# Kernel tuning notes

Measured on AMD Instinct MI355X. Metric: run time of the kernel, lower is better.

The kernel has to match this reference:

```python
import jax, jax.numpy as jnp
import numpy as np

# ---- static config (mirrors init_kwargs) ----
B, T, N, FIN = 32, 12, 500, 2
U, ND, ED = 32, 32, 2            # factor dim, node_dim, edge_dim
NRES, NDIL, NSKIP, NEND, NPRED = 32, 32, 256, 512, 12
NBLOCKS, NLAYERS, KS, ORDER = 4, 2, 2, 2
L = NBLOCKS * NLAYERS
DILATIONS = [2 ** i for _ in range(NBLOCKS) for i in range(NLAYERS)]
RF = NBLOCKS * (KS - 1) * (2 ** NLAYERS - 1) + 1  # receptive field = 13
GCIN = (ORDER * ED + 1) * NDIL                     # graph-conv concat channels = 160
BN_EPS = 1e-5


def conv1x1(x, w, b):
    # x: [B,C,N,T], w: [O,C]
    return jnp.einsum('bcnt,oc->bont', x, w) + b[None, :, None, None]


def dilated_tconv(x, w, b, d):
    # valid dilated conv along time. x: [B,C,N,T], w: [O,C,K]
    k_sz = w.shape[-1]
    t_out = x.shape[-1] - (k_sz - 1) * d
    out = jnp.einsum('bcnt,oc->bont', x[..., 0:t_out], w[..., 0])
    for k in range(1, k_sz):
        out = out + jnp.einsum('bcnt,oc->bont', x[..., k * d:k * d + t_out], w[..., k])
    return out + b[None, :, None, None]


def graph_conv(x, supports, w, b):
    # x: [B,C,N,T]; supports: [E,N,N]; diffusion over node axis (dim 2)
    out = [x]
    for e in range(supports.shape[0]):
        x1 = jnp.einsum('bcvt,vw->bcwt', x, supports[e])
        out.append(x1)
        for _ in range(ORDER - 1):
            x1 = jnp.einsum('bcvt,vw->bcwt', x1, supports[e])
            out.append(x1)
    h = jnp.concatenate(out, axis=1)  # [B,GCIN,N,T]
    return conv1x1(h, w, b)


def batchnorm(x, g, bta):
    m = x.mean(axis=(0, 2, 3), keepdims=True)
    v = ((x - m) ** 2).mean(axis=(0, 2, 3), keepdims=True)
    return (x - m) * jax.lax.rsqrt(v + BN_EPS) * g[None, :, None, None] + bta[None, :, None, None]


def _forward(inputs, factor, map_w, map_b, a1w, a1b, a2w, a2b, a3w, a3b,
             enter_w, enter_b, filt_w, filt_b, gate_w, gate_b,
             skp_w, skp_b, gc_w, gc_b, bn_g, bn_b, o1w, o1b, o2w, o2b):
    n = factor.shape[0]
    # ---- adaptive supports ----
    v = jax.nn.relu(factor @ map_w + map_b)                      # [N, ND]
    src = jnp.broadcast_to(v[None, :, :], (n, n, v.shape[1]))    # src[i,j]=v[j]
    dst = jnp.broadcast_to(v[:, None, :], (n, n, v.shape[1]))    # dst[i,j]=v[i]
    h = jnp.concatenate([src, dst], axis=-1)                     # [N,N,2*ND]
    h = jax.nn.relu(h @ a1w + a1b)
    h = jax.nn.relu(h @ a2w + a2b)
    adj = (h @ a3w + a3b).transpose(2, 0, 1)                     # [E,N,N]
    adj = jax.nn.softmax(adj, axis=2)
    supports = jnp.maximum(adj, jnp.eye(n, dtype=adj.dtype))
    # ---- input split ----
    static = jnp.einsum('btuf,pu->btpf', jnp.einsum('btnf,nu->btuf', inputs, factor), factor)
    x = jnp.concatenate([static, inputs - static], axis=-1)      # [B,T,N,2F]
    x = x.transpose(0, 3, 2, 1)                                  # [B,2F,N,T]
    t_in = x.shape[-1]
    if t_in < RF:
        x = jnp.pad(x, ((0, 0), (0, 0), (0, 0), (RF - t_in, 0)))
    x = conv1x1(x, enter_w, enter_b)                             # [B,NRES,N,RF]
    skip = jnp.zeros((x.shape[0], NSKIP, n, x.shape[-1]), dtype=x.dtype)
    # ---- stacked ST layers ----
    for i, d in enumerate(DILATIONS):
        residual = x
        f = jnp.tanh(dilated_tconv(x, filt_w[i], filt_b[i], d))
        g = jax.nn.sigmoid(dilated_tconv(x, gate_w[i], gate_b[i], d))
        x = f * g                                                # [B,NDIL,N,T']
        s = conv1x1(x, skp_w[i], skp_b[i])
        skip = skip[..., skip.shape[-1] - s.shape[-1]:] + s
        x = graph_conv(x, supports, gc_w[i], gc_b[i])
        x = x + residual[..., residual.shape[-1] - x.shape[-1]:]
        x = batchnorm(x, bn_g[i], bn_b[i])
    # ---- output head ----
    y = jax.nn.relu(skip)
    y = jax.nn.relu(conv1x1(y, o1w, o1b))
    y = conv1x1(y, o2w, o2b)                                     # [B,NPRED,N,1]
    return y, supports


def setup_inputs() -> dict:
    key = jax.random.key(0)
    ks = jax.random.split(key, 16)
    def w(i, shape, s=0.02):
        return s * jax.random.normal(ks[i], shape, dtype=jnp.float32)
    return {
        'inputs': jax.random.normal(ks[0], (B, T, N, FIN), dtype=jnp.float32),
        'factor': 0.05 * jax.random.normal(ks[1], (N, U), dtype=jnp.float32),
        'map_w': w(2, (U, ND), 0.1), 'map_b': jnp.zeros((ND,), jnp.float32),
        'a1w': w(3, (2 * ND, 2 * ND), 0.1), 'a1b': jnp.zeros((2 * ND,), jnp.float32),
        'a2w': w(4, (2 * ND, ND), 0.1), 'a2b': jnp.zeros((ND,), jnp.float32),
        'a3w': w(5, (ND, ED), 0.1), 'a3b': jnp.zeros((ED,), jnp.float32),
        'enter_w': w(6, (NRES, 2 * FIN)), 'enter_b': jnp.zeros((NRES,), jnp.float32),
        'filt_w': w(7, (L, NDIL, NRES, KS)), 'filt_b': jnp.zeros((L, NDIL), jnp.float32),
        'gate_w': w(8, (L, NDIL, NRES, KS)), 'gate_b': jnp.zeros((L, NDIL), jnp.float32),
        'skp_w': w(9, (L, NSKIP, NDIL)), 'skp_b': jnp.zeros((L, NSKIP), jnp.float32),
        'gc_w': w(10, (L, NRES, GCIN)), 'gc_b': jnp.zeros((L, NRES), jnp.float32),
        'bn_g': jnp.ones((L, NRES), jnp.float32), 'bn_b': jnp.zeros((L, NRES), jnp.float32),
        'o1w': w(11, (NEND, NSKIP)), 'o1b': jnp.zeros((NEND,), jnp.float32),
        'o2w': w(12, (NPRED, NEND)), 'o2b': jnp.zeros((NPRED,), jnp.float32),
    }


def reference(inputs, factor, map_w, map_b, a1w, a1b, a2w, a2b, a3w, a3b,
              enter_w, enter_b, filt_w, filt_b, gate_w, gate_b,
              skp_w, skp_b, gc_w, gc_b, bn_g, bn_b, o1w, o1b, o2w, o2b):
    return _forward(inputs, factor, map_w, map_b, a1w, a1b, a2w, a2b, a3w, a3b,
                    enter_w, enter_b, filt_w, filt_b, gate_w, gate_b,
                    skp_w, skp_b, gc_w, gc_b, bn_g, bn_b, o1w, o1b, o2w, o2b)
```

## Files before the change

kernel.cpp:

```cpp
#include <hip/hip_runtime.h>
#include <math.h>

#define BB 32
#define TT 12
#define NN 500
#define UU 32
#define CC 32
#define NSKIPC 256
#define NENDC 512
#define NPREDC 12
#define TX 13
#define TG 12
#define QS 384
#define VS 512
#define BNN (BB*NN)
#define DSZ (BNN*TG*CC)
#define BN_EPS 1e-5f

#define OFF_V      0u
#define OFF_ADJ    16000u
#define OFF_ASRC   516000u
#define OFF_ADST   548000u
#define OFF_PROJ   580000u
#define OFF_STAT   582048u
#define OFF_PART   582560u
#define OFF_BSUM   774560u
#define OFF_X      774816u
#define OFF_XN     7430816u
#define OFF_D      14086816u
#define OFF_GBF    38662816u
#define OFF_GLB    41734816u
#define OFF_GT     43782816u
#define OFF_ST     46928544u
#define OFF_SB     47190688u
#define OFF_ST2    47452832u
#define OFF_WSTB   47714976u
#define OFF_O1WB   47747744u
#define OFF_SKV    47813280u
#define OFF_Y1B    49861280u

typedef __attribute__((ext_vector_type(8))) short bf16x8;
typedef __attribute__((ext_vector_type(4))) float f32x4;

__device__ inline unsigned short f2bf(float f) {
  union { float f; unsigned u; } x; x.f = f;
  unsigned r = x.u + 0x7FFFu + ((x.u >> 16) & 1u);
  return (unsigned short)(r >> 16);
}
__device__ inline float bf2f(short s) {
  union { float f; unsigned u; } x;
  x.u = ((unsigned)(unsigned short)s) << 16;
  return x.f;
}
__device__ inline int pk2(float a, float b) {
  return (int)((unsigned)f2bf(a) | ((unsigned)f2bf(b) << 16));
}
__device__ inline bf16x8 pack8(f32x4 a, f32x4 b) {
  union { int i[4]; bf16x8 v; } u;
  u.i[0]=pk2(a.x,a.y); u.i[1]=pk2(a.z,a.w);
  u.i[2]=pk2(b.x,b.y); u.i[3]=pk2(b.z,b.w);
  return u.v;
}
__device__ inline f32x4 reluadd(f32x4 a, f32x4 b) {
  f32x4 r;
  r.x=fmaxf(a.x+b.x,0.f); r.y=fmaxf(a.y+b.y,0.f);
  r.z=fmaxf(a.z+b.z,0.f); r.w=fmaxf(a.w+b.w,0.f);
  return r;
}


__global__ void k_v(const float* __restrict__ factor, const float* __restrict__ map_w,
                    const float* __restrict__ map_b, float* __restrict__ v) {
  int n = blockIdx.x; int d = threadIdx.x;
  __shared__ float fr[UU];
  fr[d] = factor[n*UU + d];
  __syncthreads();
  float acc = map_b[d];
#pragma unroll
  for (int u=0;u<UU;u++) acc += fr[u]*map_w[u*32+d];
  v[n*32+d] = fmaxf(acc, 0.f);
}

__global__ void k_asrc2(const float* __restrict__ v, const float* __restrict__ a1w,
                        const float* __restrict__ a1b,
                        float* __restrict__ asrc, float* __restrict__ adst) {
  int n = blockIdx.x; int o = threadIdx.x;
  __shared__ float vn[32];
  if (o < 32) vn[o] = v[n*32+o];
  __syncthreads();
  float s = 0.f, dst = a1b[o];
#pragma unroll
  for (int u=0;u<32;u++){ s += vn[u]*a1w[u*64+o]; dst += vn[u]*a1w[(32+u)*64+o]; }
  asrc[n*64+o] = s;
  adst[n*64+o] = dst;
}

__global__ __launch_bounds__(256) void k_pair3(const float* __restrict__ asrc,
    const float* __restrict__ adst, const float* __restrict__ a2w,
    const float* __restrict__ a2b, const float* __restrict__ a3w,
    const float* __restrict__ a3b, float* __restrict__ adj) {
  int i = blockIdx.x;
  int tid = threadIdx.x;
  int wid = tid>>6, lane = tid&63;
  int lm = lane&15, g = lane>>4, lk8 = g*8;
  int jb = blockIdx.y*256 + wid*64;
  bf16x8 wf[2][2];
#pragma unroll
  for (int ks=0;ks<2;ks++)
#pragma unroll
    for (int nh=0;nh<2;nh++){
      int n = nh*16+lm;
      f32x4 lo, hi;
      lo.x=a2w[(ks*32+lk8+0)*32+n]; lo.y=a2w[(ks*32+lk8+1)*32+n];
      lo.z=a2w[(ks*32+lk8+2)*32+n]; lo.w=a2w[(ks*32+lk8+3)*32+n];
      hi.x=a2w[(ks*32+lk8+4)*32+n]; hi.y=a2w[(ks*32+lk8+5)*32+n];
      hi.z=a2w[(ks*32+lk8+6)*32+n]; hi.w=a2w[(ks*32+lk8+7)*32+n];
      wf[ks][nh] = pack8(lo, hi);
    }
  float b20 = a2b[lm], b21 = a2b[16+lm];
  float w3e0n0 = a3w[lm*2],      w3e1n0 = a3w[lm*2+1];
  float w3e0n1 = a3w[(16+lm)*2], w3e1n1 = a3w[(16+lm)*2+1];
  float b30 = a3b[0], b31 = a3b[1];
  const float* dp = adst + i*64;
  f32x4 d00 = *(const f32x4*)(dp + lk8);
  f32x4 d01 = *(const f32x4*)(dp + lk8 + 4);
  f32x4 d10 = *(const f32x4*)(dp + 32 + lk8);
  f32x4 d11 = *(const f32x4*)(dp + 32 + lk8 + 4);
#pragma unroll
  for (int mg=0; mg<4; mg++){
    int j = jb + mg*16 + lm;
    int jc = j < 500 ? j : 0;
    const float* ap = asrc + jc*64;
    f32x4 s00=*(const f32x4*)(ap+lk8),    s01=*(const f32x4*)(ap+lk8+4);
    f32x4 s10=*(const f32x4*)(ap+32+lk8), s11=*(const f32x4*)(ap+32+lk8+4);
    bf16x8 a0 = pack8(reluadd(s00,d00), reluadd(s01,d01));
    bf16x8 a1 = pack8(reluadd(s10,d10), reluadd(s11,d11));
    f32x4 acc0 = {b20,b20,b20,b20};
    f32x4 acc1 = {b21,b21,b21,b21};
    acc0 = __builtin_amdgcn_mfma_f32_16x16x32_bf16(a0, wf[0][0], acc0, 0,0,0);
    acc0 = __builtin_amdgcn_mfma_f32_16x16x32_bf16(a1, wf[1][0], acc0, 0,0,0);
    acc1 = __builtin_amdgcn_mfma_f32_16x16x32_bf16(a0, wf[0][1], acc1, 0,0,0);
    acc1 = __builtin_amdgcn_mfma_f32_16x16x32_bf16(a1, wf[1][1], acc1, 0,0,0);
    float e0[4], e1[4];
#pragma unroll
    for (int r=0;r<4;r++){
      float h2a = fmaxf(acc0[r],0.f), h2b = fmaxf(acc1[r],0.f);
      e0[r] = h2a*w3e0n0 + h2b*w3e0n1;
      e1[r] = h2a*w3e1n0 + h2b*w3e1n1;
    }
#pragma unroll
    for (int off=1; off<16; off<<=1){
#pragma unroll
      for (int r=0;r<4;r++){ e0[r]+=__shfl_xor(e0[r],off); e1[r]+=__shfl_xor(e1[r],off); }
    }
    if (lm==0){
      int j4 = jb + mg*16 + g*4;
      if (j4 < 500){
        f32x4 v0={e0[0]+b30,e0[1]+b30,e0[2]+b30,e0[3]+b30};
        f32x4 v1={e1[0]+b31,e1[1]+b31,e1[2]+b31,e1[3]+b31};
        *(f32x4*)(adj + i*500 + j4) = v0;
        *(f32x4*)(adj + 250000 + i*500 + j4) = v1;
      }
    }
  }
}

__global__ __launch_bounds__(256) void k_softmax(const float* __restrict__ adj,
    float* __restrict__ sup_out) {
  int row = blockIdx.x;
  int e = row/NN, i = row%NN;
  const float* a = adj + e*250000 + i*NN;
  __shared__ float red[64];
  float m = -1e30f;
  for (int j=threadIdx.x;j<NN;j+=256) m = fmaxf(m, a[j]);
#pragma unroll
  for (int off=32; off; off>>=1) m = fmaxf(m, __shfl_down(m, off));
  int lane = threadIdx.x & 63, wid = threadIdx.x >> 6;
  if (lane==0) red[wid]=m;
  __syncthreads();
  if (threadIdx.x==0){ float mm=red[0]; for(int w=1;w<4;w++) mm=fmaxf(mm,red[w]); red[32]=mm; }
  __syncthreads();
  m = red[32];
  float s=0.f;
  for (int j=threadIdx.x;j<NN;j+=256) s += __expf(a[j]-m);
#pragma unroll
  for (int off=32; off; off>>=1) s += __shfl_down(s, off);
  if (lane==0) red[wid]=s;
  __syncthreads();
  if (threadIdx.x==0){ float ss=0; for(int w=0;w<4;w++) ss+=red[w]; red[33]=ss; }
  __syncthreads();
  float inv = 1.f/red[33];
  for (int j=threadIdx.x;j<NN;j+=256) {
    float val = __expf(a[j]-m)*inv;
    if (j==i) val = 1.f;
    sup_out[e*250000 + i*NN + j] = val;
  }
}

__global__ __launch_bounds__(256) void k_tposeS(const float* __restrict__ sup,
    short* __restrict__ ST, short* __restrict__ SB) {
  __shared__ float ts[64][68];
  int e = blockIdx.z;
  int v0 = blockIdx.x*64, w0 = blockIdx.y*64;
  int tid = threadIdx.x;
  int vv = tid>>2, wc = (tid&3)*16;
  bool vok = (v0+vv) < 500;
#pragma unroll
  for (int c=0;c<4;c++){
    f32x4 val = {0,0,0,0};
    int wg = w0 + wc + c*4;
    if (vok && wg < 500) val = *(const f32x4*)(sup + e*250000 + (size_t)(v0+vv)*500 + wg);
    *(f32x4*)&ts[vv][wc + c*4] = val;
    int2 pv; pv.x = pk2(val.x, val.y); pv.y = pk2(val.z, val.w);
    *(int2*)(SB + (size_t)e*(512*512) + (size_t)(v0+vv)*VS + wg) = pv;
  }
  __syncthreads();
  int w = tid>>2, vc = (tid&3)*16;
  unsigned short u[16];
#pragma unroll
  for (int j=0;j<16;j++) u[j] = f2bf(ts[vc+j][w]);
  int4 o0, o1;
  o0.x = u[0]|(u[1]<<16);  o0.y = u[2]|(u[3]<<16);
  o0.z = u[4]|(u[5]<<16);  o0.w = u[6]|(u[7]<<16);
  o1.x = u[8]|(u[9]<<16);  o1.y = u[10]|(u[11]<<16);
  o1.z = u[12]|(u[13]<<16); o1.w = u[14]|(u[15]<<16);
  short* op = ST + (size_t)e*(512*512) + (size_t)(w0+w)*VS + v0 + vc;
  *(int4*)(op) = o0;
  *(int4*)(op+8) = o1;
}

__global__ __launch_bounds__(256) void k_ssq(const short* __restrict__ SB,
    const short* __restrict__ ST, short* __restrict__ ST2) {
  __shared__ __align__(16) short As[64*72];
  __shared__ __align__(16) short Bs[64*72];
  int e = blockIdx.z;
  int u0 = blockIdx.x*64, w0 = blockIdx.y*64;
  const short* Ab = SB + (size_t)e*(512*512);
  const short* Bb = ST + (size_t)e*(512*512);
  int tid = threadIdx.x;
  int row = tid>>2, col = (tid&3)*16;
  const short* ap = Ab + (size_t)(u0+row)*VS + col;
  const short* bp = Bb + (size_t)(w0+row)*VS + col;
  f32x4 ra0 = *(const f32x4*)(ap);
  f32x4 ra1 = *(const f32x4*)(ap+8);
  f32x4 rb0 = *(const f32x4*)(bp);
  f32x4 rb1 = *(const f32x4*)(bp+8);
  int wid = tid>>6, lane = tid&63;
  int wr = wid>>1, wc = wid&1;
  int lm = lane&15, lk = (lane>>4)*8;
  f32x4 acc[2][2] = {};
  short* aw = As + row*72 + col;
  short* bw = Bs + row*72 + col;
  for (int kk=0; kk<8; kk++) {
    __syncthreads();
    *(f32x4*)(aw) = ra0; *(f32x4*)(aw+8) = ra1;
    *(f32x4*)(bw) = rb0; *(f32x4*)(bw+8) = rb1;
    __syncthreads();
    if (kk < 7) {
      const short* ap2 = ap + (kk+1)*64;
      const short* bp2 = bp + (kk+1)*64;
      ra0 = *(const f32x4*)(ap2); ra1 = *(const f32x4*)(ap2+8);
      rb0 = *(const f32x4*)(bp2); rb1 = *(const f32x4*)(bp2+8);
    }
#pragma unroll
    for (int ks=0; ks<2; ks++) {
      bf16x8 af0 = *(const bf16x8*)(As + (wr*32 + lm)*72 + ks*32 + lk);
      bf16x8 af1 = *(const bf16x8*)(As + (wr*32 + 16 + lm)*72 + ks*32 + lk);
      bf16x8 bq0 = *(const bf16x8*)(Bs + (wc*32 + lm)*72 + ks*32 + lk);
      bf16x8 bq1 = *(const bf16x8*)(Bs + (wc*32 + 16 + lm)*72 + ks*32 + lk);
      acc[0][0] = __builtin_amdgcn_mfma_f32_16x16x32_bf16(af0, bq0, acc[0][0], 0,0,0);
      acc[0][1] = __builtin_amdgcn_mfma_f32_16x16x32_bf16(af0, bq1, acc[0][1], 0,0,0);
      acc[1][0] = __builtin_amdgcn_mfma_f32_16x16x32_bf16(af1, bq0, acc[1][0], 0,0,0);
      acc[1][1] = __builtin_amdgcn_mfma_f32_16x16x32_bf16(af1, bq1, acc[1][1], 0,0,0);
    }
  }
#pragma unroll
  for (int fm=0; fm<2; fm++) {
    int u4 = u0 + wr*32 + fm*16 + (lane>>4)*4;
#pragma unroll
    for (int fn=0; fn<2; fn++) {
      int w = w0 + wc*32 + fn*16 + lm;
      f32x4 v4 = acc[fm][fn];
      int2 pv; pv.x = pk2(v4.x, v4.y); pv.y = pk2(v4.z, v4.w);
      *(int2*)(ST2 + (size_t)e*(512*512) + (size_t)w*VS + u4) = pv;
    }
  }
}

__global__ __launch_bounds__(256) void k_tposeGb(const short* __restrict__ Gbf,
    short* __restrict__ GT, int qmax) {
  __shared__ __align__(16) short ts[64][72];
  int b = blockIdx.z;
  int v0 = blockIdx.x*64, q0 = blockIdx.y*64;
  int tid = threadIdx.x;
  int vv = tid>>2, qc = (tid&3)*16;
  bool ok = ((v0+vv) < 500) && ((q0+qc) < qmax);
  int4 z4 = {0,0,0,0};
  int4 i0 = z4, i1 = z4;
  if (ok){
    const short* gp = Gbf + (size_t)(b*NN + v0+vv)*QS + q0 + qc;
    i0 = *(const int4*)(gp);
    i1 = *(const int4*)(gp+8);
  }
  *(int4*)&ts[vv][qc] = i0;
  *(int4*)&ts[vv][qc+8] = i1;
  __syncthreads();
  int q = tid>>2, vc = (tid&3)*16;
  if (q0 + q < qmax) {
    unsigned short u[16];
#pragma unroll
    for (int j=0;j<16;j++) u[j] = (unsigned short)ts[vc+j][q];
    int4 o0, o1;
    o0.x = u[0]|(u[1]<<16);  o0.y = u[2]|(u[3]<<16);
    o0.z = u[4]|(u[5]<<16);  o0.w = u[6]|(u[7]<<16);
    o1.x = u[8]|(u[9]<<16);  o1.y = u[10]|(u[11]<<16);
    o1.z = u[12]|(u[13]<<16); o1.w = u[14]|(u[15]<<16);
    short* op = GT + ((size_t)b*QS + q0+q)*VS + v0 + vc;
    *(int4*)(op) = o0;
    *(int4*)(op+8) = o1;
  }
}

__global__ __launch_bounds__(256) void k_hop2(const short* __restrict__ ST,
    const short* __restrict__ ST2, const short* __restrict__ GT,
    short* __restrict__ Dout, int qmax, int qt) {
  __shared__ __align__(16) short LB[2*128*72];
  short* As = LB;
  short* Bs = LB + 128*72;
  int nwg = gridDim.x;
  int w = (blockIdx.x & 7) * (nwg >> 3) + (blockIdx.x >> 3);
  int x = w & 3; w >>= 2;
  int y = w % qt; w /= qt;
  int sel = w & 3; int b = w >> 2;
  int e = sel >> 1, hop = sel & 1;
  int w0 = x*128, q0 = y*128;
  const short* Ab = (hop ? ST2 : ST) + (size_t)e*(512*512) + (size_t)w0*VS;
  const short* Bb = GT + (size_t)b*(QS*VS) + (size_t)q0*VS;
  int tid = threadIdx.x;
  int row = tid>>2, col = (tid&3)*16;
  const short* ap0 = Ab + (size_t)row*VS + col;
  const short* ap1 = ap0 + (size_t)64*VS;
  const short* bp0 = Bb + (size_t)row*VS + col;
  const short* bp1 = bp0 + (size_t)64*VS;
  f32x4 a00=*(const f32x4*)ap0, a01=*(const f32x4*)(ap0+8);
  f32x4 a10=*(const f32x4*)ap1, a11=*(const f32x4*)(ap1+8);
  f32x4 b00=*(const f32x4*)bp0, b01=*(const f32x4*)(bp0+8);
  f32x4 b10=*(const f32x4*)bp1, b11=*(const f32x4*)(bp1+8);
  int wid = tid>>6, lane = tid&63;
  int wr = wid>>1, wc = wid&1;
  int lm = lane&15, lk = (lane>>4)*8;
  f32x4 acc[4][4] = {};
  short* aw0 = As + row*72 + col; short* aw1 = aw0 + 64*72;
  short* bw0 = Bs + row*72 + col; short* bw1 = bw0 + 64*72;
  for (int kk=0; kk<8; kk++) {
    __syncthreads();
    *(f32x4*)(aw0) = a00; *(f32x4*)(aw0+8) = a01;
    *(f32x4*)(aw1) = a10; *(f32x4*)(aw1+8) = a11;
    *(f32x4*)(bw0) = b00; *(f32x4*)(bw0+8) = b01;
    *(f32x4*)(bw1) = b10; *(f32x4*)(bw1+8) = b11;
    __syncthreads();
    if (kk < 7) {
      int o = (kk+1)*64;
      a00=*(const f32x4*)(ap0+o); a01=*(const f32x4*)(ap0+o+8);
      a10=*(const f32x4*)(ap1+o); a11=*(const f32x4*)(ap1+o+8);
      b00=*(const f32x4*)(bp0+o); b01=*(const f32x4*)(bp0+o+8);
      b10=*(const f32x4*)(bp1+o); b11=*(const f32x4*)(bp1+o+8);
    }
#pragma unroll
    for (int ks=0; ks<2; ks++) {
      bf16x8 af[4], bq[4];
#pragma unroll
      for (int fm=0;fm<4;fm++) af[fm] = *(const bf16x8*)(As + (wr*64+fm*16+lm)*72 + ks*32 + lk);
#pragma unroll
      for (int fn=0;fn<4;fn++) bq[fn] = *(const bf16x8*)(Bs + (wc*64+fn*16+lm)*72 + ks*32 + lk);
#pragma unroll
      for (int fm=0;fm<4;fm++)
#pragma unroll
        for (int fn=0;fn<4;fn++)
          acc[fm][fn] = __builtin_amdgcn_mfma_f32_16x16x32_bf16(af[fm], bq[fn], acc[fm][fn], 0,0,0);
    }
  }
  __syncthreads();
#pragma unroll
  for (int fm=0; fm<4; fm++){
    int rr = wr*64 + fm*16 + (lane>>4)*4;
#pragma unroll
    for (int fn=0; fn<4; fn++){
      int cc = wc*64 + fn*16 + lm;
      f32x4 v4 = acc[fm][fn];
      LB[(rr+0)*136 + cc] = (short)f2bf(v4.x);
      LB[(rr+1)*136 + cc] = (short)f2bf(v4.y);
      LB[(rr+2)*136 + cc] = (short)f2bf(v4.z);
      LB[(rr+3)*136 + cc] = (short)f2bf(v4.w);
    }
  }
  __syncthreads();
  short* Ob = Dout + (size_t)sel*DSZ + (size_t)b*(NN*QS);
#pragma unroll
  for (int pass=0; pass<8; pass++){
    int rr = pass*16 + (tid>>4);
    int cc = (tid&15)*8;
    int wg = w0 + rr, qg = q0 + cc;
    if (wg < 500 && qg < qmax){
      int4 vv = *(const int4*)(LB + rr*136 + cc);
      *(int4*)(Ob + (size_t)wg*QS + qg) = vv;
    }
  }
}


__global__ void k_proj(const float* __restrict__ inputs, const float* __restrict__ factor,
                       float* __restrict__ proj) {
  int bt = blockIdx.x;
  __shared__ float xin[NN*2];
  for (int idx=threadIdx.x; idx<NN*2; idx+=64) xin[idx] = inputs[bt*NN*2 + idx];
  __syncthreads();
  int u = threadIdx.x>>1, f = threadIdx.x&1;
  float acc=0.f;
  for (int n=0;n<NN;n++) acc += xin[n*2+f]*factor[n*UU+u];
  proj[bt*64 + u*2+f] = acc;
}

__global__ __launch_bounds__(256) void k_enter(const float* __restrict__ inputs,
    const float* __restrict__ factor, const float* __restrict__ proj,
    const float* __restrict__ ew, const float* __restrict__ eb, float* __restrict__ X) {
  int idx = blockIdx.x*256+threadIdx.x;
  if (idx >= BB*NN*TX) return;
  int t = idx % TX; int n = (idx/TX)%NN; int b = idx/(TX*NN);
  float x4[4]={0.f,0.f,0.f,0.f};
  if (t>0) {
    int tt=t-1;
    float s0=0.f,s1=0.f;
    const float* pr = proj + (b*TT+tt)*64;
    const float* fr = factor + n*UU;
#pragma unroll
    for(int u=0;u<UU;u++){ s0 += pr[u*2]*fr[u]; s1 += pr[u*2+1]*fr[u]; }
    float i0 = inputs[((b*TT+tt)*NN+n)*2];
    float i1 = inputs[((b*TT+tt)*NN+n)*2+1];
    x4[0]=s0; x4[1]=s1; x4[2]=i0-s0; x4[3]=i1-s1;
  }
  float* xp = X + ((size_t)(b*NN+n)*TX + t)*CC;
#pragma unroll
  for(int o=0;o<CC;o++){
    xp[o] = eb[o] + ew[o*4]*x4[0] + ew[o*4+1]*x4[1] + ew[o*4+2]*x4[2] + ew[o*4+3]*x4[3];
  }
}


__global__ __launch_bounds__(256) void k_gated3(const float* __restrict__ X,
    short* __restrict__ Gbf, short* __restrict__ Glb,
    const float* __restrict__ fw, const float* __restrict__ fb,
    const float* __restrict__ gw, const float* __restrict__ gb,
    const float* __restrict__ stat, int use_stat, int d, int t_out, int lidx) {
  __shared__ __align__(16) short As[64*72];
  __shared__ __align__(16) short Wb[64*72];
  __shared__ float scs[32], shs[32];
  int tid = threadIdx.x;
  if (tid < 32) {
    scs[tid] = use_stat ? stat[tid] : 1.0f;
    shs[tid] = use_stat ? stat[32 + tid] : 0.0f;
  }
  for (int i = tid; i < 2048; i += 256) {
    int o = i >> 6, k = i & 63;
    Wb[o*72 + k]      = (short)f2bf(fw[i]);
    Wb[(32+o)*72 + k] = (short)f2bf(gw[i]);
  }
  __syncthreads();
  int m0 = blockIdx.x * 64;
  {
    int mm = tid & 63;
    int kb = (tid >> 6) * 16;
    int c0 = kb >> 1;
    int m = m0 + mm;
    int bn = m / t_out, t = m - bn * t_out;
    const float* xr = X + (size_t)bn * (TX * CC);
    float4 a0 = *(const float4*)(xr + t * 32 + c0);
    float4 a1 = *(const float4*)(xr + t * 32 + c0 + 4);
    float4 b0 = *(const float4*)(xr + (t + d) * 32 + c0);
    float4 b1 = *(const float4*)(xr + (t + d) * 32 + c0 + 4);
    float va[8] = {a0.x,a0.y,a0.z,a0.w,a1.x,a1.y,a1.z,a1.w};
    float vb[8] = {b0.x,b0.y,b0.z,b0.w,b1.x,b1.y,b1.z,b1.w};
    int iv[8];
#pragma unroll
    for (int j = 0; j < 8; j++) {
      float sc = scs[c0+j], sh = shs[c0+j];
      iv[j] = pk2(va[j]*sc + sh, vb[j]*sc + sh);
    }
    int4 w0 = {iv[0],iv[1],iv[2],iv[3]};
    int4 w1 = {iv[4],iv[5],iv[6],iv[7]};
    *(int4*)(As + mm*72 + kb) = w0;
    *(int4*)(As + mm*72 + kb + 8) = w1;
  }
  __syncthreads();
  int wid = tid>>6, lane = tid&63;
  int lm = lane&15, g = lane>>4, lk8 = g*8;
  f32x4 acc[4] = {};
#pragma unroll
  for (int kk=0; kk<2; kk++){
    bf16x8 af = *(const bf16x8*)(As + (wid*16+lm)*72 + kk*32 + lk8);
#pragma unroll
    for (int fn=0; fn<4; fn++){
      bf16x8 bq = *(const bf16x8*)(Wb + (fn*16+lm)*72 + kk*32 + lk8);
      acc[fn] = __builtin_amdgcn_mfma_f32_16x16x32_bf16(af, bq, acc[fn], 0,0,0);
    }
  }
#pragma unroll
  for (int fn=0; fn<2; fn++){
    int o = fn*16 + lm;
    float fbv = fb[o], gbv = gb[o];
#pragma unroll
    for (int r=0; r<4; r++){
      int m = m0 + wid*16 + g*4 + r;
      int bn = m / t_out, t = m - bn*t_out;
      float f = acc[fn][r] + fbv;
      float gg = acc[fn+2][r] + gbv;
      float th = 2.f/(1.f+__expf(-2.f*f)) - 1.f;
      float sg = 1.f/(1.f+__expf(-gg));
      unsigned short ov = f2bf(th*sg);
      Gbf[(size_t)bn*QS + t*32 + o] = (short)ov;
      if (t == t_out-1) Glb[(size_t)bn*256 + lidx*32 + o] = (short)ov;
    }
  }
}


template<int TOUT>
__global__ __launch_bounds__(256) void k_gc3(const short* __restrict__ Gbf,
    const short* __restrict__ Dbf, const float* __restrict__ Xc, float* __restrict__ Xn,
    const float* __restrict__ gcw, const float* __restrict__ gcb,
    const float* __restrict__ stat, int use_stat, float* __restrict__ part, int d) {
  int tid = threadIdx.x;
  int wid = tid>>6, lane = tid&63;
  int lm = lane&15, g = lane>>4, lk8 = g*8;
  int m0 = blockIdx.x*256 + wid*64;
  const int M = 16000*TOUT;
  float* pp = part + ((size_t)blockIdx.x*4 + wid)*64;
  if (m0 >= M){
    if (lane < 16){ pp[lane]=0.f; pp[16+lane]=0.f; pp[32+lane]=0.f; pp[48+lane]=0.f; }
    return;
  }
  bf16x8 wf[5][2];
#pragma unroll
  for (int ks=0;ks<5;ks++)
#pragma unroll
    for (int nh=0;nh<2;nh++){
      const float* wp = gcw + (nh*16+lm)*160 + ks*32 + lk8;
      wf[ks][nh] = pack8(*(const f32x4*)wp, *(const f32x4*)(wp+4));
    }
  float scn0 = use_stat ? stat[lm]    : 1.f;
  float scn1 = use_stat ? stat[16+lm] : 1.f;
  float shn0 = use_stat ? stat[32+lm] : 0.f;
  float shn1 = use_stat ? stat[48+lm] : 0.f;
  float gb0 = gcb[lm], gb1 = gcb[16+lm];
  float ss0=0.f, sq0=0.f, ss1=0.f, sq1=0.f;
#pragma unroll
  for (int mg=0; mg<4; mg++){
    int m = m0 + mg*16 + lm;
    int bn = m / TOUT; int t = m - bn*TOUT;
    size_t off = (size_t)bn*(TG*CC) + t*32 + lk8;
    f32x4 acc0={0,0,0,0}, acc1={0,0,0,0};
    {
      bf16x8 af = *(const bf16x8*)(Gbf + off);
      acc0 = __builtin_amdgcn_mfma_f32_16x16x32_bf16(af, wf[0][0], acc0, 0,0,0);
      acc1 = __builtin_amdgcn_mfma_f32_16x16x32_bf16(af, wf[0][1], acc1, 0,0,0);
    }
#pragma unroll
    for (int ks=1;ks<5;ks++){
      bf16x8 af = *(const bf16x8*)(Dbf + (size_t)(ks-1)*DSZ + off);
      acc0 = __builtin_amdgcn_mfma_f32_16x16x32_bf16(af, wf[ks][0], acc0, 0,0,0);
      acc1 = __builtin_amdgcn_mfma_f32_16x16x32_bf16(af, wf[ks][1], acc1, 0,0,0);
    }
#pragma unroll
    for (int r=0;r<4;r++){
      int mr = m0 + mg*16 + g*4 + r;
      int bnr = mr / TOUT; int tr = mr - bnr*TOUT;
      size_t xoff = (size_t)bnr*(TX*CC);
      float r0 = Xc[xoff + (tr+d)*32 + lm];
      float r1 = Xc[xoff + (tr+d)*32 + 16 + lm];
      float v0 = acc0[r] + gb0 + r0*scn0 + shn0;
      float v1 = acc1[r] + gb1 + r1*scn1 + shn1;
      Xn[xoff + tr*32 + lm] = v0;
      Xn[xoff + tr*32 + 16 + lm] = v1;
      ss0+=v0; sq0+=v0*v0; ss1+=v1; sq1+=v1*v1;
    }
  }
#pragma unroll
  for (int off=16; off<64; off<<=1){
    ss0+=__shfl_xor(ss0,off); sq0+=__shfl_xor(sq0,off);
    ss1+=__shfl_xor(ss1,off); sq1+=__shfl_xor(sq1,off);
  }
  if (lane<16){
    pp[lane]=ss0; pp[16+lane]=ss1; pp[32+lane]=sq0; pp[48+lane]=sq1;
  }
}

__global__ __launch_bounds__(64) void k_stat2a(const float* __restrict__ part, int nblk,
    float* __restrict__ part2) {
  int t = threadIdx.x;
  float s = 0.f;
  for (int i = blockIdx.x; i < nblk; i += 64) s += part[(size_t)i*64 + t];
  part2[blockIdx.x*64 + t] = s;
}

__global__ __launch_bounds__(64) void k_stat2b(const float* __restrict__ part2,
    const float* __restrict__ g, const float* __restrict__ b,
    float* __restrict__ statout, float cntinv) {
  int t = threadIdx.x;
  float s = 0.f;
#pragma unroll 8
  for (int i = 0; i < 64; i++) s += part2[i*64 + t];
  __shared__ float red[64];
  red[t] = s;
  __syncthreads();
  if (t < 32){
    float sum = red[t], sq = red[32+t];
    float m = sum*cntinv, var = sq*cntinv - m*m;
    float sc = rsqrtf(var + BN_EPS)*g[t];
    statout[t] = sc;
    statout[32+t] = b[t] - m*sc;
  }
}


__global__ void k_wstack2(const float* __restrict__ skp_w, const float* __restrict__ skp_b,
                          const float* __restrict__ o1w,
                          short* __restrict__ Wstb, short* __restrict__ o1wb,
                          float* __restrict__ bsum) {
  int bid = blockIdx.x;
  int idx = bid*256 + threadIdx.x;
  if (bid < 256){
    int kk = idx >> 8, o = idx & 255;
    Wstb[o*256 + kk] = (short)f2bf(skp_w[(kk>>5)*8192 + o*32 + (kk&31)]);
    if (idx < 256){
      float s=0.f;
      for (int l=0;l<8;l++) s += skp_b[l*256+idx];
      bsum[idx]=s;
    }
  } else {
    int j = idx - 65536;
    o1wb[j] = (short)f2bf(o1w[j]);
  }
}

__global__ __launch_bounds__(256) void k_mm(const short* __restrict__ A,
    const short* __restrict__ B, const float* __restrict__ bias,
    short* __restrict__ out, int ldout, int K) {
  __shared__ __align__(16) short As[64*72];
  __shared__ __align__(16) short Bs[64*72];
  int m0 = blockIdx.x*64, n0 = blockIdx.y*64;
  int tid = threadIdx.x;
  int row = tid>>2, col = (tid&3)*16;
  const short* ap = A + (size_t)(m0+row)*K + col;
  const short* bp = B + (size_t)(n0+row)*K + col;
  f32x4 ra0 = *(const f32x4*)(ap);
  f32x4 ra1 = *(const f32x4*)(ap+8);
  f32x4 rb0 = *(const f32x4*)(bp);
  f32x4 rb1 = *(const f32x4*)(bp+8);
  int wid = tid>>6, lane = tid&63;
  int wr = wid>>1, wc = wid&1;
  int lm = lane&15, lk = (lane>>4)*8;
  f32x4 acc[2][2] = {};
  short* aw = As + row*72 + col;
  short* bw = Bs + row*72 + col;
  int nk = K>>6;
  for (int kk=0; kk<nk; kk++) {
    __syncthreads();
    *(f32x4*)(aw) = ra0; *(f32x4*)(aw+8) = ra1;
    *(f32x4*)(bw) = rb0; *(f32x4*)(bw+8) = rb1;
    __syncthreads();
    if (kk < nk-1) {
      const short* ap2 = ap + (kk+1)*64;
      const short* bp2 = bp + (kk+1)*64;
      ra0 = *(const f32x4*)(ap2); ra1 = *(const f32x4*)(ap2+8);
      rb0 = *(const f32x4*)(bp2); rb1 = *(const f32x4*)(bp2+8);
    }
#pragma unroll
    for (int ks=0; ks<2; ks++) {
      bf16x8 af0 = *(const bf16x8*)(As + (wr*32 + lm)*72 + ks*32 + lk);
      bf16x8 af1 = *(const bf16x8*)(As + (wr*32 + 16 + lm)*72 + ks*32 + lk);
      bf16x8 bq0 = *(const bf16x8*)(Bs + (wc*32 + lm)*72 + ks*32 + lk);
      bf16x8 bq1 = *(const bf16x8*)(Bs + (wc*32 + 16 + lm)*72 + ks*32 + lk);
      acc[0][0] = __builtin_amdgcn_mfma_f32_16x16x32_bf16(af0, bq0, acc[0][0], 0,0,0);
      acc[0][1] = __builtin_amdgcn_mfma_f32_16x16x32_bf16(af0, bq1, acc[0][1], 0,0,0);
      acc[1][0] = __builtin_amdgcn_mfma_f32_16x16x32_bf16(af1, bq0, acc[1][0], 0,0,0);
      acc[1][1] = __builtin_amdgcn_mfma_f32_16x16x32_bf16(af1, bq1, acc[1][1], 0,0,0);
    }
  }
#pragma unroll
  for (int fm=0; fm<2; fm++) {
    int mb = m0 + wr*32 + fm*16 + (lane>>4)*4;
#pragma unroll
    for (int fn=0; fn<2; fn++) {
      int n = n0 + wc*32 + fn*16 + lm;
      float bv = bias[n];
      f32x4 v4 = acc[fm][fn];
#pragma unroll
      for (int r=0;r<4;r++)
        out[(size_t)(mb+r)*ldout + n] = (short)f2bf(fmaxf(v4[r]+bv, 0.f));
    }
  }
}

__global__ __launch_bounds__(256) void k_head2m(const short* __restrict__ Y1b,
    const float* __restrict__ o2w, const float* __restrict__ o2b, float* __restrict__ y) {
  int tid = threadIdx.x;
  int wid = tid>>6, lane = tid&63;
  int lm = lane&15, g = lane>>4, lk8 = g*8;
  int m0 = blockIdx.x*64 + wid*16;
  bf16x8 wf[16];
#pragma unroll
  for (int ks=0; ks<16; ks++){
    f32x4 lo={0,0,0,0}, hi={0,0,0,0};
    if (lm < NPREDC){
      const float* wp = o2w + lm*NENDC + ks*32 + lk8;
      lo = *(const f32x4*)wp; hi = *(const f32x4*)(wp+4);
    }
    wf[ks] = pack8(lo, hi);
  }
  f32x4 acc = {0,0,0,0};
  const short* ar = Y1b + (size_t)(m0+lm)*NENDC;
#pragma unroll
  for (int ks=0; ks<16; ks++){
    bf16x8 af = *(const bf16x8*)(ar + ks*32 + lk8);
    acc = __builtin_amdgcn_mfma_f32_16x16x32_bf16(af, wf[ks], acc, 0,0,0);
  }
  int p = lm;
  if (p < NPREDC){
    float bv = o2b[p];
#pragma unroll
    for (int r=0;r<4;r++){
      int m = m0 + g*4 + r;
      int bb = m/NN, n = m - bb*NN;
      y[(bb*NPREDC+p)*NN + n] = acc[r] + bv;
    }
  }
}


extern "C" void kernel_launch(void* const* d_in, const int* in_sizes, int n_in,
                              void* d_out, int out_size, void* d_ws, size_t ws_size,
                              hipStream_t stream) {
  const float* inputs  = (const float*)d_in[0];
  const float* factor  = (const float*)d_in[1];
  const float* map_w   = (const float*)d_in[2];
  const float* map_b   = (const float*)d_in[3];
  const float* a1w     = (const float*)d_in[4];
  const float* a1b     = (const float*)d_in[5];
  const float* a2w     = (const float*)d_in[6];
  const float* a2b     = (const float*)d_in[7];
  const float* a3w     = (const float*)d_in[8];
  const float* a3b     = (const float*)d_in[9];
  const float* enter_w = (const float*)d_in[10];
  const float* enter_b = (const float*)d_in[11];
  const float* filt_w  = (const float*)d_in[12];
  const float* filt_b  = (const float*)d_in[13];
  const float* gate_w  = (const float*)d_in[14];
  const float* gate_b  = (const float*)d_in[15];
  const float* skp_w   = (const float*)d_in[16];
  const float* skp_b   = (const float*)d_in[17];
  const float* gc_w    = (const float*)d_in[18];
  const float* gc_b    = (const float*)d_in[19];
  const float* bn_g    = (const float*)d_in[20];
  const float* bn_b    = (const float*)d_in[21];
  const float* o1w     = (const float*)d_in[22];
  const float* o1b     = (const float*)d_in[23];
  const float* o2w     = (const float*)d_in[24];
  const float* o2b     = (const float*)d_in[25];
  (void)in_sizes; (void)n_in; (void)out_size; (void)ws_size;

  float* ws = (float*)d_ws;
  float* v      = ws + OFF_V;
  float* adj    = ws + OFF_ADJ;
  float* part2  = ws + OFF_ADJ;
  float* asrc   = ws + OFF_ASRC;
  float* adst   = ws + OFF_ADST;
  float* proj   = ws + OFF_PROJ;
  float* statb  = ws + OFF_STAT;
  float* part   = ws + OFF_PART;
  float* bsum   = ws + OFF_BSUM;
  float* X      = ws + OFF_X;
  float* Xn     = ws + OFF_XN;
  short* Dbf    = (short*)(ws + OFF_D);
  short* Gbf    = (short*)(ws + OFF_GBF);
  short* Glb    = (short*)(ws + OFF_GLB);
  short* GT     = (short*)(ws + OFF_GT);
  short* ST     = (short*)(ws + OFF_ST);
  short* SB     = (short*)(ws + OFF_SB);
  short* ST2    = (short*)(ws + OFF_ST2);
  short* Wstb   = (short*)(ws + OFF_WSTB);
  short* o1wb   = (short*)(ws + OFF_O1WB);
  short* skvb   = (short*)(ws + OFF_SKV);
  short* Y1b    = (short*)(ws + OFF_Y1B);

  float* y_out   = (float*)d_out;
  float* sup_out = y_out + BB*NPREDC*NN;

  k_v<<<NN, 32, 0, stream>>>(factor, map_w, map_b, v);
  k_asrc2<<<NN, 64, 0, stream>>>(v, a1w, a1b, asrc, adst);
  {
    dim3 gp(NN, 2);
    k_pair3<<<gp, 256, 0, stream>>>(asrc, adst, a2w, a2b, a3w, a3b, adj);
  }
  k_softmax<<<2*NN, 256, 0, stream>>>(adj, sup_out);
  {
    dim3 gt(8, 8, 2);
    k_tposeS<<<gt, 256, 0, stream>>>(sup_out, ST, SB);
    k_ssq<<<gt, 256, 0, stream>>>(SB, ST, ST2);
  }

  k_proj<<<BB*TT, 64, 0, stream>>>(inputs, factor, proj);
  k_enter<<<(BB*NN*TX+255)/256, 256, 0, stream>>>(inputs, factor, proj, enter_w, enter_b, X);

  k_wstack2<<<768, 256, 0, stream>>>(skp_w, skp_b, o1w, Wstb, o1wb, bsum);

  float* Xc = X; float* Xo = Xn;
  int t = TX;
  static const int dil[8]={1,2,1,2,1,2,1,2};
  for (int l=0;l<7;l++){
    int d=dil[l], t_out=t-d;
    const float* st = statb + (l>0 ? (l-1)*64 : 0);
    k_gated3<<<250*t_out,256,0,stream>>>(Xc, Gbf, Glb, filt_w + l*2048, filt_b + l*32,
                                         gate_w + l*2048, gate_b + l*32, st, l>0, d, t_out, l);
    int qmax = t_out*CC;
    int qt64 = (qmax+63)/64;
    dim3 gtp(8, qt64, 32);
    k_tposeGb<<<gtp,256,0,stream>>>(Gbf, GT, qmax);
    int qt128 = (qmax+127)/128;
    k_hop2<<<512*qt128,256,0,stream>>>(ST, ST2, GT, Dbf, qmax, qt128);
    int nb = (16000*t_out + 255)/256;
    const float* gcwl = gc_w + l*5120;
    const float* gcbl = gc_b + l*32;
    switch (t_out){
      case 12: k_gc3<12><<<nb,256,0,stream>>>(Gbf,Dbf,Xc,Xo,gcwl,gcbl,st,l>0,part,d); break;
      case 10: k_gc3<10><<<nb,256,0,stream>>>(Gbf,Dbf,Xc,Xo,gcwl,gcbl,st,l>0,part,d); break;
      case  9: k_gc3< 9><<<nb,256,0,stream>>>(Gbf,Dbf,Xc,Xo,gcwl,gcbl,st,l>0,part,d); break;
      case  7: k_gc3< 7><<<nb,256,0,stream>>>(Gbf,Dbf,Xc,Xo,gcwl,gcbl,st,l>0,part,d); break;
      case  6: k_gc3< 6><<<nb,256,0,stream>>>(Gbf,Dbf,Xc,Xo,gcwl,gcbl,st,l>0,part,d); break;
      case  4: k_gc3< 4><<<nb,256,0,stream>>>(Gbf,Dbf,Xc,Xo,gcwl,gcbl,st,l>0,part,d); break;
      default: k_gc3< 3><<<nb,256,0,stream>>>(Gbf,Dbf,Xc,Xo,gcwl,gcbl,st,l>0,part,d); break;
    }
    k_stat2a<<<64,64,0,stream>>>(part, nb*4, part2);
    k_stat2b<<<1,64,0,stream>>>(part2, bn_g + l*32, bn_b + l*32,
                                statb + l*64, 1.f/(16000.f*(float)t_out));
    float* tmp=Xc; Xc=Xo; Xo=tmp;
    t = t_out;
  }
  k_gated3<<<250*1,256,0,stream>>>(Xc, Gbf, Glb, filt_w + 7*2048, filt_b + 7*32,
                                   gate_w + 7*2048, gate_b + 7*32, statb + 6*64, 1, 2, 1, 7);

  {
    dim3 gs(BNN/64, NSKIPC/64);
    k_mm<<<gs,256,0,stream>>>(Glb, Wstb, bsum, skvb, NSKIPC, 256);
    dim3 gh(BNN/64, NENDC/64);
    k_mm<<<gh,256,0,stream>>>(skvb, o1wb, o1b, Y1b, NENDC, 256);
    k_head2m<<<BNN/64,256,0,stream>>>(Y1b, o2w, o2b, y_out);
  }
}
```

Baseline: 728.7 us.

## Fuse graph diffusion GEMMs with 1x1 graph-conv mixing and BN stats

Replaces the separate diffusion kernel (which wrote four bf16 diffusion tensors to global memory) and the graph-conv channel-mix kernel with one fused kernel. Each workgroup computes both hops for each support on a 128-node by 64-column tile, stages the results in shared memory, and immediately multiplies them by the graph-conv weights. It then adds the residual and writes per-block BN partial sums. This removes a large global write and read of the diffusion outputs, but it uses more shared memory, uses narrower q-tiles (64 instead of 128), drops register prefetch double buffering, and reloads the weights in every block.

```diff
diff --git a/kernel.cpp b/kernel.cpp
--- a/kernel.cpp
+++ b/kernel.cpp
@@ -321,90 +321,179 @@
   }
 }
 
-__global__ __launch_bounds__(256) void k_hop2(const short* __restrict__ ST,
+__global__ __launch_bounds__(256) void k_fuse(const short* __restrict__ ST,
     const short* __restrict__ ST2, const short* __restrict__ GT,
-    short* __restrict__ Dout, int qmax, int qt) {
-  __shared__ __align__(16) short LB[2*128*72];
-  short* As = LB;
-  short* Bs = LB + 128*72;
+    const short* __restrict__ Gbf, const float* __restrict__ Xc,
+    float* __restrict__ Xn, const float* __restrict__ gcw,
+    const float* __restrict__ gcb, const float* __restrict__ stat, int use_stat,
+    float* __restrict__ part, int d, int qt, int qmax) {
+  __shared__ __align__(16) short SH[3*128*72];
+  __shared__ __align__(16) short gws[5*32*32];
+  __shared__ float red[4][64];
+  short* As0 = SH;
+  short* As1 = SH + 128*72;
+  short* Bs  = SH + 2*128*72;
+  short* mixb = SH;
   int nwg = gridDim.x;
-  int w = (blockIdx.x & 7) * (nwg >> 3) + (blockIdx.x >> 3);
-  int x = w & 3; w >>= 2;
-  int y = w % qt; w /= qt;
-  int sel = w & 3; int b = w >> 2;
-  int e = sel >> 1, hop = sel & 1;
-  int w0 = x*128, q0 = y*128;
-  const short* Ab = (hop ? ST2 : ST) + (size_t)e*(512*512) + (size_t)w0*VS;
-  const short* Bb = GT + (size_t)b*(QS*VS) + (size_t)q0*VS;
-  int tid = threadIdx.x;
-  int row = tid>>2, col = (tid&3)*16;
-  const short* ap0 = Ab + (size_t)row*VS + col;
-  const short* ap1 = ap0 + (size_t)64*VS;
-  const short* bp0 = Bb + (size_t)row*VS + col;
-  const short* bp1 = bp0 + (size_t)64*VS;
-  f32x4 a00=*(const f32x4*)ap0, a01=*(const f32x4*)(ap0+8);
-  f32x4 a10=*(const f32x4*)ap1, a11=*(const f32x4*)(ap1+8);
-  f32x4 b00=*(const f32x4*)bp0, b01=*(const f32x4*)(bp0+8);
-  f32x4 b10=*(const f32x4*)bp1, b11=*(const f32x4*)(bp1+8);
-  int wid = tid>>6, lane = tid&63;
-  int wr = wid>>1, wc = wid&1;
-  int lm = lane&15, lk = (lane>>4)*8;
-  f32x4 acc[4][4] = {};
-  short* aw0 = As + row*72 + col; short* aw1 = aw0 + 64*72;
-  short* bw0 = Bs + row*72 + col; short* bw1 = bw0 + 64*72;
-  for (int kk=0; kk<8; kk++) {
-    __syncthreads();
-    *(f32x4*)(aw0) = a00; *(f32x4*)(aw0+8) = a01;
-    *(f32x4*)(aw1) = a10; *(f32x4*)(aw1+8) = a11;
-    *(f32x4*)(bw0) = b00; *(f32x4*)(bw0+8) = b01;
-    *(f32x4*)(bw1) = b10; *(f32x4*)(bw1+8) = b11;
-    __syncthreads();
-    if (kk < 7) {
-      int o = (kk+1)*64;
-      a00=*(const f32x4*)(ap0+o); a01=*(const f32x4*)(ap0+o+8);
-      a10=*(const f32x4*)(ap1+o); a11=*(const f32x4*)(ap1+o+8);
-      b00=*(const f32x4*)(bp0+o); b01=*(const f32x4*)(bp0+o+8);
-      b10=*(const f32x4*)(bp1+o); b11=*(const f32x4*)(bp1+o+8);
-    }
-#pragma unroll
-    for (int ks=0; ks<2; ks++) {
-      bf16x8 af[4], bq[4];
-#pragma unroll
-      for (int fm=0;fm<4;fm++) af[fm] = *(const bf16x8*)(As + (wr*64+fm*16+lm)*72 + ks*32 + lk);
-#pragma unroll
-      for (int fn=0;fn<4;fn++) bq[fn] = *(const bf16x8*)(Bs + (wc*64+fn*16+lm)*72 + ks*32 + lk);
-#pragma unroll
-      for (int fm=0;fm<4;fm++)
-#pragma unroll
-        for (int fn=0;fn<4;fn++)
-          acc[fm][fn] = __builtin_amdgcn_mfma_f32_16x16x32_bf16(af[fm], bq[fn], acc[fm][fn], 0,0,0);
-    }
-  }
-  __syncthreads();
-#pragma unroll
-  for (int fm=0; fm<4; fm++){
-    int rr = wr*64 + fm*16 + (lane>>4)*4;
-#pragma unroll
-    for (int fn=0; fn<4; fn++){
-      int cc = wc*64 + fn*16 + lm;
-      f32x4 v4 = acc[fm][fn];
-      LB[(rr+0)*136 + cc] = (short)f2bf(v4.x);
-      LB[(rr+1)*136 + cc] = (short)f2bf(v4.y);
-      LB[(rr+2)*136 + cc] = (short)f2bf(v4.z);
-      LB[(rr+3)*136 + cc] = (short)f2bf(v4.w);
-    }
-  }
-  __syncthreads();
-  short* Ob = Dout + (size_t)sel*DSZ + (size_t)b*(NN*QS);
-#pragma unroll
-  for (int pass=0; pass<8; pass++){
-    int rr = pass*16 + (tid>>4);
-    int cc = (tid&15)*8;
-    int wg = w0 + rr, qg = q0 + cc;
-    if (wg < 500 && qg < qmax){
-      int4 vv = *(const int4*)(LB + rr*136 + cc);
-      *(int4*)(Ob + (size_t)wg*QS + qg) = vv;
-    }
+  int v = (blockIdx.x & 7)*(nwg>>3) + (blockIdx.x>>3);
+  int x = v & 3; v >>= 2;
+  int y = v % qt; int b = v / qt;
+  int w0 = x*128, q0 = y*64;
+  int tid = threadIdx.x, wid = tid>>6, lane = tid&63;
+  int lm = lane&15, g = lane>>4, lk8 = g*8;
+  for (int i = tid; i < 5120; i += 256){
+    int src = i >> 10, rem = i & 1023;
+    int cp = rem >> 5, c = rem & 31;
+    gws[i] = (short)f2bf(gcw[cp*160 + src*32 + c]);
+  }
+  f32x4 outa[2][2][2] = {};
+
+#define MIX_STEP(SRC) do { \
+  _Pragma("unroll") \
+  for (int mf=0; mf<2; mf++) \
+    _Pragma("unroll") \
+    for (int t=0; t<2; t++) { \
+      bf16x8 af = *(const bf16x8*)(mixb + (wid*32+mf*16+lm)*72 + t*32 + lk8); \
+      _Pragma("unroll") \
+      for (int nf=0; nf<2; nf++) { \
+        bf16x8 bq = *(const bf16x8*)(gws + (SRC)*1024 + (nf*16+lm)*32 + lk8); \
+        outa[mf][t][nf] = __builtin_amdgcn_mfma_f32_16x16x32_bf16(af, bq, outa[mf][t][nf], 0,0,0); \
+      } \
+    } \
+} while(0)
+
+  {
+#pragma unroll
+    for (int p=0;p<4;p++){
+      int rr = (tid>>3) + p*32, cc = (tid&7)*8;
+      int4 z = {0,0,0,0};
+      if (w0+rr < 500 && q0+cc < qmax)
+        z = *(const int4*)(Gbf + (size_t)(b*NN + w0+rr)*QS + q0 + cc);
+      *(int4*)(mixb + rr*72 + cc) = z;
+    }
+    __syncthreads();
+    MIX_STEP(0);
+    __syncthreads();
+  }
+
+  int arow = tid>>2, acol = (tid&3)*16;
+#pragma unroll
+  for (int e=0; e<2; e++){
+    const short* A0b = ST  + (size_t)e*(512*512) + (size_t)w0*VS;
+    const short* A1b = ST2 + (size_t)e*(512*512) + (size_t)w0*VS;
+    const short* Bb  = GT + (size_t)b*(QS*VS) + (size_t)q0*VS;
+    f32x4 acc0[2][4] = {}, acc1[2][4] = {};
+    for (int kk=0; kk<8; kk++){
+      const short* a0 = A0b + (size_t)arow*VS + kk*64 + acol;
+      const short* a1 = A1b + (size_t)arow*VS + kk*64 + acol;
+      const short* bp = Bb + (size_t)arow*VS + kk*64 + acol;
+      int4 r00 = *(const int4*)a0;
+      int4 r01 = *(const int4*)(a0+8);
+      int4 r02 = *(const int4*)(a0 + (size_t)64*VS);
+      int4 r03 = *(const int4*)(a0 + (size_t)64*VS + 8);
+      int4 r10 = *(const int4*)a1;
+      int4 r11 = *(const int4*)(a1+8);
+      int4 r12 = *(const int4*)(a1 + (size_t)64*VS);
+      int4 r13 = *(const int4*)(a1 + (size_t)64*VS + 8);
+      int4 rb0 = *(const int4*)bp;
+      int4 rb1 = *(const int4*)(bp+8);
+      __syncthreads();
+      *(int4*)(As0 + arow*72 + acol) = r00;
+      *(int4*)(As0 + arow*72 + acol + 8) = r01;
+      *(int4*)(As0 + (arow+64)*72 + acol) = r02;
+      *(int4*)(As0 + (arow+64)*72 + acol + 8) = r03;
+      *(int4*)(As1 + arow*72 + acol) = r10;
+      *(int4*)(As1 + arow*72 + acol + 8) = r11;
+      *(int4*)(As1 + (arow+64)*72 + acol) = r12;
+      *(int4*)(As1 + (arow+64)*72 + acol + 8) = r13;
+      *(int4*)(Bs + arow*72 + acol) = rb0;
+      *(int4*)(Bs + arow*72 + acol + 8) = rb1;
+      __syncthreads();
+#pragma unroll
+      for (int ks=0; ks<2; ks++){
+        bf16x8 bq[4];
+#pragma unroll
+        for (int nf=0; nf<4; nf++) bq[nf] = *(const bf16x8*)(Bs + (nf*16+lm)*72 + ks*32 + lk8);
+#pragma unroll
+        for (int mf=0; mf<2; mf++){
+          bf16x8 af0 = *(const bf16x8*)(As0 + (wid*32+mf*16+lm)*72 + ks*32 + lk8);
+          bf16x8 af1 = *(const bf16x8*)(As1 + (wid*32+mf*16+lm)*72 + ks*32 + lk8);
+#pragma unroll
+          for (int nf=0; nf<4; nf++){
+            acc0[mf][nf] = __builtin_amdgcn_mfma_f32_16x16x32_bf16(af0, bq[nf], acc0[mf][nf], 0,0,0);
+            acc1[mf][nf] = __builtin_amdgcn_mfma_f32_16x16x32_bf16(af1, bq[nf], acc1[mf][nf], 0,0,0);
+          }
+        }
+      }
+    }
+    __syncthreads();
+#pragma unroll
+    for (int mf=0; mf<2; mf++)
+#pragma unroll
+      for (int nf=0; nf<4; nf++){
+        f32x4 vv = acc0[mf][nf];
+        int rbase = (wid*32+mf*16+g*4)*72 + nf*16+lm;
+        mixb[rbase]       = (short)f2bf(vv.x);
+        mixb[rbase+72]    = (short)f2bf(vv.y);
+        mixb[rbase+144]   = (short)f2bf(vv.z);
+        mixb[rbase+216]   = (short)f2bf(vv.w);
+      }
+    __syncthreads();
+    MIX_STEP(1+e*2);
+    __syncthreads();
+#pragma unroll
+    for (int mf=0; mf<2; mf++)
+#pragma unroll
+      for (int nf=0; nf<4; nf++){
+        f32x4 vv = acc1[mf][nf];
+        int rbase = (wid*32+mf*16+g*4)*72 + nf*16+lm;
+        mixb[rbase]       = (short)f2bf(vv.x);
+        mixb[rbase+72]    = (short)f2bf(vv.y);
+        mixb[rbase+144]   = (short)f2bf(vv.z);
+        mixb[rbase+216]   = (short)f2bf(vv.w);
+      }
+    __syncthreads();
+    MIX_STEP(2+e*2);
+    __syncthreads();
+  }
+#undef MIX_STEP
+
+  float scn0 = use_stat ? stat[lm]    : 1.f;
+  float scn1 = use_stat ? stat[16+lm] : 1.f;
+  float shn0 = use_stat ? stat[32+lm] : 0.f;
+  float shn1 = use_stat ? stat[48+lm] : 0.f;
+  float gb0 = gcb[lm], gb1 = gcb[16+lm];
+  float ss0=0.f, ss1=0.f, sq0=0.f, sq1=0.f;
+  int tbase = q0>>5;
+#pragma unroll
+  for (int mf=0; mf<2; mf++)
+#pragma unroll
+    for (int t=0; t<2; t++){
+      if (q0 + t*32 >= qmax) continue;
+      int tg = tbase + t;
+#pragma unroll
+      for (int r=0; r<4; r++){
+        int w = w0 + wid*32 + mf*16 + g*4 + r;
+        if (w >= 500) continue;
+        size_t xoff = (size_t)(b*NN + w)*(TX*CC);
+        float v0 = outa[mf][t][0][r] + gb0 + Xc[xoff + (tg+d)*32 + lm]*scn0 + shn0;
+        float v1 = outa[mf][t][1][r] + gb1 + Xc[xoff + (tg+d)*32 + 16+lm]*scn1 + shn1;
+        Xn[xoff + tg*32 + lm] = v0;
+        Xn[xoff + tg*32 + 16+lm] = v1;
+        ss0+=v0; sq0+=v0*v0; ss1+=v1; sq1+=v1*v1;
+      }
+    }
+#pragma unroll
+  for (int off=16; off<64; off<<=1){
+    ss0+=__shfl_xor(ss0,off); sq0+=__shfl_xor(sq0,off);
+    ss1+=__shfl_xor(ss1,off); sq1+=__shfl_xor(sq1,off);
+  }
+  if (lane<16){
+    red[wid][lm]=ss0; red[wid][16+lm]=ss1; red[wid][32+lm]=sq0; red[wid][48+lm]=sq1;
+  }
+  __syncthreads();
+  if (tid<64){
+    part[(size_t)blockIdx.x*64 + tid] = red[0][tid]+red[1][tid]+red[2][tid]+red[3][tid];
   }
 }
 
@@ -520,77 +609,6 @@
       Gbf[(size_t)bn*QS + t*32 + o] = (short)ov;
       if (t == t_out-1) Glb[(size_t)bn*256 + lidx*32 + o] = (short)ov;
     }
-  }
-}
-
-
-template<int TOUT>
-__global__ __launch_bounds__(256) void k_gc3(const short* __restrict__ Gbf,
-    const short* __restrict__ Dbf, const float* __restrict__ Xc, float* __restrict__ Xn,
-    const float* __restrict__ gcw, const float* __restrict__ gcb,
-    const float* __restrict__ stat, int use_stat, float* __restrict__ part, int d) {
-  int tid = threadIdx.x;
-  int wid = tid>>6, lane = tid&63;
-  int lm = lane&15, g = lane>>4, lk8 = g*8;
-  int m0 = blockIdx.x*256 + wid*64;
-  const int M = 16000*TOUT;
-  float* pp = part + ((size_t)blockIdx.x*4 + wid)*64;
-  if (m0 >= M){
-    if (lane < 16){ pp[lane]=0.f; pp[16+lane]=0.f; pp[32+lane]=0.f; pp[48+lane]=0.f; }
-    return;
-  }
-  bf16x8 wf[5][2];
-#pragma unroll
-  for (int ks=0;ks<5;ks++)
-#pragma unroll
-    for (int nh=0;nh<2;nh++){
-      const float* wp = gcw + (nh*16+lm)*160 + ks*32 + lk8;
-      wf[ks][nh] = pack8(*(const f32x4*)wp, *(const f32x4*)(wp+4));
-    }
-  float scn0 = use_stat ? stat[lm]    : 1.f;
-  float scn1 = use_stat ? stat[16+lm] : 1.f;
-  float shn0 = use_stat ? stat[32+lm] : 0.f;
-  float shn1 = use_stat ? stat[48+lm] : 0.f;
-  float gb0 = gcb[lm], gb1 = gcb[16+lm];
-  float ss0=0.f, sq0=0.f, ss1=0.f, sq1=0.f;
-#pragma unroll
-  for (int mg=0; mg<4; mg++){
-    int m = m0 + mg*16 + lm;
-    int bn = m / TOUT; int t = m - bn*TOUT;
-    size_t off = (size_t)bn*(TG*CC) + t*32 + lk8;
-    f32x4 acc0={0,0,0,0}, acc1={0,0,0,0};
-    {
-      bf16x8 af = *(const bf16x8*)(Gbf + off);
-      acc0 = __builtin_amdgcn_mfma_f32_16x16x32_bf16(af, wf[0][0], acc0, 0,0,0);
-      acc1 = __builtin_amdgcn_mfma_f32_16x16x32_bf16(af, wf[0][1], acc1, 0,0,0);
-    }
-#pragma unroll
-    for (int ks=1;ks<5;ks++){
-      bf16x8 af = *(const bf16x8*)(Dbf + (size_t)(ks-1)*DSZ + off);
-      acc0 = __builtin_amdgcn_mfma_f32_16x16x32_bf16(af, wf[ks][0], acc0, 0,0,0);
-      acc1 = __builtin_amdgcn_mfma_f32_16x16x32_bf16(af, wf[ks][1], acc1, 0,0,0);
-    }
-#pragma unroll
-    for (int r=0;r<4;r++){
-      int mr = m0 + mg*16 + g*4 + r;
-      int bnr = mr / TOUT; int tr = mr - bnr*TOUT;
-      size_t xoff = (size_t)bnr*(TX*CC);
-      float r0 = Xc[xoff + (tr+d)*32 + lm];
-      float r1 = Xc[xoff + (tr+d)*32 + 16 + lm];
-      float v0 = acc0[r] + gb0 + r0*scn0 + shn0;
-      float v1 = acc1[r] + gb1 + r1*scn1 + shn1;
-      Xn[xoff + tr*32 + lm] = v0;
-      Xn[xoff + tr*32 + 16 + lm] = v1;
-      ss0+=v0; sq0+=v0*v0; ss1+=v1; sq1+=v1*v1;
-    }
-  }
-#pragma unroll
-  for (int off=16; off<64; off<<=1){
-    ss0+=__shfl_xor(ss0,off); sq0+=__shfl_xor(sq0,off);
-    ss1+=__shfl_xor(ss1,off); sq1+=__shfl_xor(sq1,off);
-  }
-  if (lane<16){
-    pp[lane]=ss0; pp[16+lane]=ss1; pp[32+lane]=sq0; pp[48+lane]=sq1;
   }
 }
 
@@ -780,7 +798,6 @@
   float* bsum   = ws + OFF_BSUM;
   float* X      = ws + OFF_X;
   float* Xn     = ws + OFF_XN;
-  short* Dbf    = (short*)(ws + OFF_D);
   short* Gbf    = (short*)(ws + OFF_GBF);
   short* Glb    = (short*)(ws + OFF_GLB);
   short* GT     = (short*)(ws + OFF_GT);
@@ -825,21 +842,11 @@
     int qt64 = (qmax+63)/64;
     dim3 gtp(8, qt64, 32);
     k_tposeGb<<<gtp,256,0,stream>>>(Gbf, GT, qmax);
-    int qt128 = (qmax+127)/128;
-    k_hop2<<<512*qt128,256,0,stream>>>(ST, ST2, GT, Dbf, qmax, qt128);
-    int nb = (16000*t_out + 255)/256;
-    const float* gcwl = gc_w + l*5120;
-    const float* gcbl = gc_b + l*32;
-    switch (t_out){
-      case 12: k_gc3<12><<<nb,256,0,stream>>>(Gbf,Dbf,Xc,Xo,gcwl,gcbl,st,l>0,part,d); break;
-      case 10: k_gc3<10><<<nb,256,0,stream>>>(Gbf,Dbf,Xc,Xo,gcwl,gcbl,st,l>0,part,d); break;
-      case  9: k_gc3< 9><<<nb,256,0,stream>>>(Gbf,Dbf,Xc,Xo,gcwl,gcbl,st,l>0,part,d); break;
-      case  7: k_gc3< 7><<<nb,256,0,stream>>>(Gbf,Dbf,Xc,Xo,gcwl,gcbl,st,l>0,part,d); break;
-      case  6: k_gc3< 6><<<nb,256,0,stream>>>(Gbf,Dbf,Xc,Xo,gcwl,gcbl,st,l>0,part,d); break;
-      case  4: k_gc3< 4><<<nb,256,0,stream>>>(Gbf,Dbf,Xc,Xo,gcwl,gcbl,st,l>0,part,d); break;
-      default: k_gc3< 3><<<nb,256,0,stream>>>(Gbf,Dbf,Xc,Xo,gcwl,gcbl,st,l>0,part,d); break;
-    }
-    k_stat2a<<<64,64,0,stream>>>(part, nb*4, part2);
+    int nwg = 4*qt64*32;
+    k_fuse<<<nwg,256,0,stream>>>(ST, ST2, GT, Gbf, Xc, Xo,
+                                 gc_w + l*5120, gc_b + l*32, st, l>0,
+                                 part, d, qt64, qmax);
+    k_stat2a<<<64,64,0,stream>>>(part, nwg, part2);
     k_stat2b<<<1,64,0,stream>>>(part2, bn_g + l*32, bn_b + l*32,
                                 statb + l*64, 1.f/(16000.f*(float)t_out));
     float* tmp=Xc; Xc=Xo; Xo=tmp;
```

Result: no change. 725.0 us (-0.5%).
